# Optimization experiments

Measured on AMD Instinct MI355X. Metric: run time of the kernel, lower is better.

## Reference

```python
import jax, jax.numpy as jnp
import numpy as np

B, L, HID, NH = 4, 1024, 768, 12
D = HID // NH  # 64 per-head
SCALE = 1.0 / np.sqrt(D).astype(np.float32)
NEG = -1e15


def layer_norm(x, g, b, eps=1e-5):
    m = x.mean(-1, keepdims=True)
    v = ((x - m) ** 2).mean(-1, keepdims=True)
    return (x - m) / jnp.sqrt(v + eps) * g + b


def setup_inputs() -> dict:
    key = jax.random.key(0)
    ks = jax.random.split(key, 20)
    s = 0.02
    inp = jax.random.normal(ks[0], (B, L, HID), jnp.float32)
    seq_len = jax.random.randint(ks[1], (B,), 1, L + 1).astype(jnp.int32)
    rel_pos_embedding = jax.random.normal(ks[2], (B, NH, L, L), jnp.float32)
    def lin(k):
        k1, k2 = jax.random.split(k)
        W = jax.random.normal(k1, (HID, HID), jnp.float32) * s  # stored [in,out]
        b = jax.random.normal(k2, (HID,), jnp.float32) * s
        return W, b
    Wq, bq = lin(ks[3])
    Wk, bk = lin(ks[4])
    Wv, bv = lin(ks[5])
    Wo, bo = lin(ks[6])  # attn ff_final
    W0, b0 = lin(ks[7])  # FFN layer 0 (ff_size == hidden_size)
    W1, b1 = lin(ks[8])  # FFN layer 1
    ln_g = jnp.ones((HID,), jnp.float32)
    ln_b = jnp.zeros((HID,), jnp.float32)
    return {"inp": inp, "seq_len": seq_len, "lex_num": 0,
            "rel_pos_embedding": rel_pos_embedding,
            "Wq": Wq, "bq": bq, "Wk": Wk, "bk": bk, "Wv": Wv, "bv": bv,
            "Wo": Wo, "bo": bo, "W0": W0, "b0": b0, "W1": W1, "b1": b1,
            "ln_g": ln_g, "ln_b": ln_b}


def reference(inp, seq_len, lex_num, rel_pos_embedding,
              Wq, bq, Wk, bk, Wv, bv, Wo, bo, W0, b0, W1, b1, ln_g, ln_b):
    # layer_preprocess: '' -> identity
    x = inp
    # --- attention (q=k=v=x) ---
    q = (x @ Wq + bq).reshape(B, L, NH, D)
    k = (x @ Wk + bk).reshape(B, L, NH, D)
    v = (x @ Wv + bv).reshape(B, L, NH, D)
    scores = jnp.einsum('blhd,bmhd->bhlm', q, k) * SCALE + rel_pos_embedding
    valid = jnp.arange(L)[None, :] < (seq_len + lex_num)[:, None]  # [B,L]
    scores = jnp.where(valid[:, None, None, :], scores, NEG)
    attn = jax.nn.softmax(scores, axis=-1)  # attn dropout: eval mode -> identity
    ctx = jnp.einsum('bhlm,bmhd->blhd', attn, v).reshape(B, L, HID)
    y = ctx @ Wo + bo  # ff_final
    # layer_postprocess 'an': output = output + inp(of process); then LayerNorm
    y = layer_norm(y + y, ln_g, ln_b)
    # layer_preprocess '' -> identity, then FFN [hid, hid, hid]
    h = y @ W0 + b0
    h = jax.nn.relu(h)
    h = h @ W1 + b1
    out = layer_norm(h + h, ln_g, ln_b)
    return out
```

## Files before the change

kernel.cpp:

```cpp
#include <hip/hip_runtime.h>
#include <math.h>

#define B_   4
#define L_   1024
#define HID_ 768
#define NH_  12
#define D_   64
#define SCALE_ 0.125f
#define NEGV (-1e15f)

typedef __attribute__((ext_vector_type(4))) float  f32x4;
typedef __attribute__((ext_vector_type(8))) __bf16 bf16x8;
typedef __attribute__((ext_vector_type(8))) unsigned short ushort8v;
typedef __attribute__((ext_vector_type(4))) unsigned short ushort4v;

typedef const __attribute__((address_space(1))) unsigned int* gas1_t;
typedef __attribute__((address_space(3))) unsigned int*       las3_t;
#define GLDS16(g, l) __builtin_amdgcn_global_load_lds((gas1_t)(g), (las3_t)(l), 16, 0, 0)

static __device__ __forceinline__ unsigned short f2bf(float f) {
    unsigned int u = __builtin_bit_cast(unsigned int, f);
    u += 0x7fffu + ((u >> 16) & 1u);
    return (unsigned short)(u >> 16);
}

__global__ __launch_bounds__(256) void convert_x_kernel(
    const float* __restrict__ in, unsigned short* __restrict__ out, int n4)
{
    int i = blockIdx.x * 256 + threadIdx.x;
    if (i < n4) {
        float4 v = reinterpret_cast<const float4*>(in)[i];
        ushort4v o;
        o.x = f2bf(v.x); o.y = f2bf(v.y); o.z = f2bf(v.z); o.w = f2bf(v.w);
        reinterpret_cast<ushort4v*>(out)[i] = o;
    }
}

struct WArgs { const float* w[6]; unsigned short* wt[6]; };

__global__ __launch_bounds__(256) void transpose_w_kernel(WArgs a)
{
    const float* W = a.w[blockIdx.z];
    unsigned short* Wt = a.wt[blockIdx.z];
    __shared__ float t[64][65];
    const int tid = threadIdx.x;
    const int lr = tid >> 2, lc4 = (tid & 3) * 16;
    const int r0 = blockIdx.y * 64, c0 = blockIdx.x * 64;
#pragma unroll
    for (int j = 0; j < 4; ++j) {
        float4 v = *reinterpret_cast<const float4*>(&W[(size_t)(r0 + lr) * HID_ + c0 + lc4 + j * 4]);
        t[lr][lc4 + j * 4 + 0] = v.x;
        t[lr][lc4 + j * 4 + 1] = v.y;
        t[lr][lc4 + j * 4 + 2] = v.z;
        t[lr][lc4 + j * 4 + 3] = v.w;
    }
    __syncthreads();
    unsigned short tmp[16];
#pragma unroll
    for (int j = 0; j < 16; ++j) tmp[j] = f2bf(t[lc4 + j][lr]);
    unsigned short* dst = &Wt[(size_t)(c0 + lr) * HID_ + r0 + lc4];
    *reinterpret_cast<ushort8v*>(dst)     = *reinterpret_cast<ushort8v*>(&tmp[0]);
    *reinterpret_cast<ushort8v*>(dst + 8) = *reinterpret_cast<ushort8v*>(&tmp[8]);
}

struct GemmJob {
    const unsigned short* A;
    const unsigned short* Wt;
    const float* bias;
    void* C;
    int mode;
    int relu;
    float scale;
};
struct GemmArgs { GemmJob j[3]; };

__global__ __launch_bounds__(256, 4) void gemm_bf16_kernel(GemmArgs args)
{
    const GemmJob jb = args.j[blockIdx.z];
    __shared__ unsigned short As[64 * 64];
    __shared__ unsigned short Bs[128 * 64];

    const int tid = threadIdx.x;
    const int w = tid >> 6, lane = tid & 63, g = lane >> 4, lq = lane & 15;
    const int m0 = blockIdx.x * 64, n0 = blockIdx.y * 128;

    f32x4 acc[4][2];
#pragma unroll
    for (int i = 0; i < 4; ++i)
#pragma unroll
        for (int j = 0; j < 2; ++j) acc[i][j] = (f32x4){0.f, 0.f, 0.f, 0.f};

    const int sr = tid >> 3;
    const int kq = ((tid & 7) ^ (sr & 7)) * 8;
    const unsigned short* Ap0 = jb.A  + (size_t)(m0 + sr) * HID_ + kq;
    const unsigned short* Ap1 = jb.A  + (size_t)(m0 + 32 + sr) * HID_ + kq;
    const unsigned short* Bp0 = jb.Wt + (size_t)(n0 + sr) * HID_ + kq;
    const unsigned short* Bp1 = jb.Wt + (size_t)(n0 + 32 + sr) * HID_ + kq;
    const unsigned short* Bp2 = jb.Wt + (size_t)(n0 + 64 + sr) * HID_ + kq;
    const unsigned short* Bp3 = jb.Wt + (size_t)(n0 + 96 + sr) * HID_ + kq;
    char* AsB = (char*)As;
    char* BsB = (char*)Bs;
    const int wb = w * 1024;

    for (int k0 = 0; k0 < HID_; k0 += 64) {
        __syncthreads();
        GLDS16(Ap0 + k0, AsB + wb);
        GLDS16(Ap1 + k0, AsB + 4096 + wb);
        GLDS16(Bp0 + k0, BsB + wb);
        GLDS16(Bp1 + k0, BsB + 4096 + wb);
        GLDS16(Bp2 + k0, BsB + 8192 + wb);
        GLDS16(Bp3 + k0, BsB + 12288 + wb);
        __syncthreads();

#pragma unroll
        for (int ks = 0; ks < 2; ++ks) {
            bf16x8 af[4], bf[2];
#pragma unroll
            for (int mi = 0; mi < 4; ++mi) {
                int row = mi * 16 + lq;
                int c = (ks * 4 + g) ^ (row & 7);
                af[mi] = *reinterpret_cast<const bf16x8*>(&As[row * 64 + c * 8]);
            }
#pragma unroll
            for (int ni = 0; ni < 2; ++ni) {
                int row = w * 32 + ni * 16 + lq;
                int c = (ks * 4 + g) ^ (row & 7);
                bf[ni] = *reinterpret_cast<const bf16x8*>(&Bs[row * 64 + c * 8]);
            }
            __builtin_amdgcn_s_setprio(1);
#pragma unroll
            for (int mi = 0; mi < 4; ++mi)
#pragma unroll
                for (int ni = 0; ni < 2; ++ni)
                    acc[mi][ni] = __builtin_amdgcn_mfma_f32_16x16x32_bf16(
                        af[mi], bf[ni], acc[mi][ni], 0, 0, 0);
            __builtin_amdgcn_s_setprio(0);
        }
    }

    float bcol[2];
#pragma unroll
    for (int ni = 0; ni < 2; ++ni) bcol[ni] = jb.bias[n0 + w * 32 + ni * 16 + lq];

#pragma unroll
    for (int mi = 0; mi < 4; ++mi) {
#pragma unroll
        for (int ni = 0; ni < 2; ++ni) {
            const int n = n0 + w * 32 + ni * 16 + lq;
            float v[4];
#pragma unroll
            for (int r = 0; r < 4; ++r) {
                float x = (acc[mi][ni][r] + bcol[ni]) * jb.scale;
                if (jb.relu) x = fmaxf(x, 0.f);
                v[r] = x;
            }
            const int mbase = m0 + mi * 16 + 4 * g;
            if (jb.mode == 0) {
                float* C = (float*)jb.C;
#pragma unroll
                for (int r = 0; r < 4; ++r)
                    C[(size_t)(mbase + r) * HID_ + n] = v[r];
            } else if (jb.mode == 1) {
                unsigned short* C = (unsigned short*)jb.C;
#pragma unroll
                for (int r = 0; r < 4; ++r)
                    C[(size_t)(mbase + r) * HID_ + n] = f2bf(v[r]);
            } else {
                unsigned short* C = (unsigned short*)jb.C;
                const int bb = mbase >> 10, ltok = mbase & 1023;
                ushort4v o;
                o.x = f2bf(v[0]); o.y = f2bf(v[1]); o.z = f2bf(v[2]); o.w = f2bf(v[3]);
                *reinterpret_cast<ushort4v*>(&C[(size_t)(bb * HID_ + n) * L_ + ltok]) = o;
            }
        }
    }
}

__global__ __launch_bounds__(256, 3) void attn_mfma_kernel(
    const unsigned short* __restrict__ Qb, const unsigned short* __restrict__ Kb,
    const unsigned short* __restrict__ Vtb, const float* __restrict__ rel,
    const int* __restrict__ seq_len, const int* __restrict__ lex_num,
    unsigned short* __restrict__ ctx)
{
    const int qt = blockIdx.x, bh = blockIdx.y;
    const int b = bh / NH_, h = bh % NH_;
    const int q0 = qt * 64;
    const int sl = seq_len[b] + lex_num[0];
    const int nkt = (sl + 63) >> 6;

    __shared__ unsigned short Ks0[64 * 72], Ks1[64 * 72];
    __shared__ unsigned short Vs0[64 * 72], Vs1[64 * 72];
    __shared__ unsigned short Ps[64 * 72];

    const int tid = threadIdx.x;
    const int w = tid >> 6, lane = tid & 63, g = lane >> 4, lq = lane & 15;
    const int r0 = tid >> 3, cc0 = tid & 7;
    const int r1 = 32 + r0;

    const unsigned short* Kbase = Kb  + (size_t)(b * L_) * HID_ + h * D_;
    const unsigned short* Vbase = Vtb + (size_t)(b * HID_ + h * D_) * L_;
    const float* relbase = rel + (size_t)bh * (L_ * L_) + (size_t)(q0 + w * 16 + 4 * g) * L_ + lq;

    bf16x8 aq[2];
#pragma unroll
    for (int ks = 0; ks < 2; ++ks)
        aq[ks] = *reinterpret_cast<const bf16x8*>(
            &Qb[(size_t)(b * L_ + q0 + w * 16 + lq) * HID_ + h * D_ + ks * 32 + g * 8]);

    f32x4 acc[4];
    float m_r[4], l_r[4];
#pragma unroll
    for (int i = 0; i < 4; ++i) {
        acc[i] = (f32x4){0.f, 0.f, 0.f, 0.f};
        m_r[i] = -3e38f; l_r[i] = 0.f;
    }

    ushort8v kA0, kA1, vA0, vA1, kB0, kB1, vB0, vB1;
    float relA[16], relB[16];

    auto load_set = [&](int kt_, ushort8v& K0, ushort8v& K1, ushort8v& V0,
                        ushort8v& V1, float (&R)[16]) {
        const int k0 = kt_ * 64;
        K0 = *reinterpret_cast<const ushort8v*>(&Kbase[(size_t)(k0 + r0) * HID_ + cc0 * 8]);
        K1 = *reinterpret_cast<const ushort8v*>(&Kbase[(size_t)(k0 + r1) * HID_ + cc0 * 8]);
        V0 = *reinterpret_cast<const ushort8v*>(&Vbase[(size_t)r0 * L_ + k0 + cc0 * 8]);
        V1 = *reinterpret_cast<const ushort8v*>(&Vbase[(size_t)r1 * L_ + k0 + cc0 * 8]);
#pragma unroll
        for (int ni = 0; ni < 4; ++ni)
#pragma unroll
            for (int r = 0; r < 4; ++r)
                R[ni * 4 + r] = relbase[(size_t)r * L_ + k0 + ni * 16];
    };

    auto body = [&](int kt_, ushort8v& K0, ushort8v& K1, ushort8v& V0, ushort8v& V1,
                    float (&R)[16], unsigned short* KsC, unsigned short* VsC) {
        const int k0 = kt_ * 64;
        *reinterpret_cast<ushort8v*>(&KsC[r0 * 72 + cc0 * 8]) = K0;
        *reinterpret_cast<ushort8v*>(&KsC[r1 * 72 + cc0 * 8]) = K1;
        *reinterpret_cast<ushort8v*>(&VsC[r0 * 72 + cc0 * 8]) = V0;
        *reinterpret_cast<ushort8v*>(&VsC[r1 * 72 + cc0 * 8]) = V1;
        __syncthreads();

        {
            int tn = kt_ + 2; if (tn > nkt - 1) tn = nkt - 1;
            const int kn = tn * 64;
            K0 = *reinterpret_cast<const ushort8v*>(&Kbase[(size_t)(kn + r0) * HID_ + cc0 * 8]);
            K1 = *reinterpret_cast<const ushort8v*>(&Kbase[(size_t)(kn + r1) * HID_ + cc0 * 8]);
            V0 = *reinterpret_cast<const ushort8v*>(&Vbase[(size_t)r0 * L_ + kn + cc0 * 8]);
            V1 = *reinterpret_cast<const ushort8v*>(&Vbase[(size_t)r1 * L_ + kn + cc0 * 8]);
        }

        f32x4 s[4];
#pragma unroll
        for (int ni = 0; ni < 4; ++ni) s[ni] = (f32x4){0.f, 0.f, 0.f, 0.f};
        __builtin_amdgcn_s_setprio(1);
#pragma unroll
        for (int ks = 0; ks < 2; ++ks) {
#pragma unroll
            for (int ni = 0; ni < 4; ++ni) {
                bf16x8 bk = *reinterpret_cast<const bf16x8*>(
                    &KsC[(ni * 16 + lq) * 72 + ks * 32 + g * 8]);
                s[ni] = __builtin_amdgcn_mfma_f32_16x16x32_bf16(aq[ks], bk, s[ni], 0, 0, 0);
            }
        }
        __builtin_amdgcn_s_setprio(0);

        float sv[4][4];
#pragma unroll
        for (int ni = 0; ni < 4; ++ni) {
            const int col = k0 + ni * 16 + lq;
            const bool ok = col < sl;
#pragma unroll
            for (int r = 0; r < 4; ++r)
                sv[ni][r] = ok ? (s[ni][r] + R[ni * 4 + r]) : NEGV;
        }

        {
            int tn = kt_ + 2; if (tn > nkt - 1) tn = nkt - 1;
            const int kn = tn * 64;
#pragma unroll
            for (int ni = 0; ni < 4; ++ni)
#pragma unroll
                for (int r = 0; r < 4; ++r)
                    R[ni * 4 + r] = relbase[(size_t)r * L_ + kn + ni * 16];
        }

#pragma unroll
        for (int r = 0; r < 4; ++r) {
            float rm = fmaxf(fmaxf(sv[0][r], sv[1][r]), fmaxf(sv[2][r], sv[3][r]));
            rm = fmaxf(rm, __shfl_xor(rm, 1, 16));
            rm = fmaxf(rm, __shfl_xor(rm, 2, 16));
            rm = fmaxf(rm, __shfl_xor(rm, 4, 16));
            rm = fmaxf(rm, __shfl_xor(rm, 8, 16));
            float mn = fmaxf(m_r[r], rm);
            float sc = __expf(m_r[r] - mn);
            float p[4], rs = 0.f;
#pragma unroll
            for (int ni = 0; ni < 4; ++ni) {
                p[ni] = __expf(sv[ni][r] - mn);
                rs += p[ni];
            }
            rs += __shfl_xor(rs, 1, 16);
            rs += __shfl_xor(rs, 2, 16);
            rs += __shfl_xor(rs, 4, 16);
            rs += __shfl_xor(rs, 8, 16);
            l_r[r] = l_r[r] * sc + rs;
            m_r[r] = mn;
#pragma unroll
            for (int ni = 0; ni < 4; ++ni) {
                acc[ni][r] *= sc;
                Ps[(w * 16 + 4 * g + r) * 72 + ni * 16 + lq] = f2bf(p[ni]);
            }
        }

        __builtin_amdgcn_s_setprio(1);
#pragma unroll
        for (int ks = 0; ks < 2; ++ks) {
            bf16x8 ap = *reinterpret_cast<const bf16x8*>(
                &Ps[(w * 16 + lq) * 72 + ks * 32 + g * 8]);
#pragma unroll
            for (int ni = 0; ni < 4; ++ni) {
                bf16x8 bv = *reinterpret_cast<const bf16x8*>(
                    &VsC[(ni * 16 + lq) * 72 + ks * 32 + g * 8]);
                acc[ni] = __builtin_amdgcn_mfma_f32_16x16x32_bf16(ap, bv, acc[ni], 0, 0, 0);
            }
        }
        __builtin_amdgcn_s_setprio(0);
    };

    load_set(0, kA0, kA1, vA0, vA1, relA);
    load_set(nkt > 1 ? 1 : 0, kB0, kB1, vB0, vB1, relB);

    for (int kt = 0; kt < nkt; kt += 2) {
        body(kt, kA0, kA1, vA0, vA1, relA, Ks0, Vs0);
        if (kt + 1 < nkt)
            body(kt + 1, kB0, kB1, vB0, vB1, relB, Ks1, Vs1);
    }

    float inv[4];
#pragma unroll
    for (int r = 0; r < 4; ++r) inv[r] = 1.f / l_r[r];
#pragma unroll
    for (int ni = 0; ni < 4; ++ni)
#pragma unroll
        for (int r = 0; r < 4; ++r)
            ctx[(size_t)(b * L_ + q0 + w * 16 + 4 * g + r) * HID_ + h * D_ + ni * 16 + lq] =
                f2bf(acc[ni][r] * inv[r]);
}

__global__ __launch_bounds__(256) void ln2_kernel(
    const float* __restrict__ in, const float* __restrict__ g,
    const float* __restrict__ bta, void* __restrict__ out, int bf16out)
{
    const int row = blockIdx.x;
    const float* x = in + (size_t)row * HID_;
    const int tid = threadIdx.x;

    float vals[3];
    float s = 0.f, ss = 0.f;
#pragma unroll
    for (int j = 0; j < 3; ++j) {
        float t = 2.f * x[tid + j * 256];
        vals[j] = t;
        s += t;
        ss += t * t;
    }
#pragma unroll
    for (int m = 1; m < 64; m <<= 1) {
        s += __shfl_xor(s, m, 64);
        ss += __shfl_xor(ss, m, 64);
    }
    __shared__ float sb[4], ssb[4];
    if ((tid & 63) == 0) { sb[tid >> 6] = s; ssb[tid >> 6] = ss; }
    __syncthreads();
    s = sb[0] + sb[1] + sb[2] + sb[3];
    ss = ssb[0] + ssb[1] + ssb[2] + ssb[3];
    const float mean = s * (1.f / 768.f);
    float var = ss * (1.f / 768.f) - mean * mean;
    if (var < 0.f) var = 0.f;
    const float invs = rsqrtf(var + 1e-5f);
    if (bf16out) {
        unsigned short* o = (unsigned short*)out;
#pragma unroll
        for (int j = 0; j < 3; ++j) {
            int c = tid + j * 256;
            o[(size_t)row * HID_ + c] = f2bf((vals[j] - mean) * invs * g[c] + bta[c]);
        }
    } else {
        float* o = (float*)out;
#pragma unroll
        for (int j = 0; j < 3; ++j) {
            int c = tid + j * 256;
            o[(size_t)row * HID_ + c] = (vals[j] - mean) * invs * g[c] + bta[c];
        }
    }
}

extern "C" void kernel_launch(void* const* d_in, const int* in_sizes, int n_in,
                              void* d_out, int out_size, void* d_ws, size_t ws_size,
                              hipStream_t stream) {
    const float* inp     = (const float*)d_in[0];
    const int*   seq_len = (const int*)d_in[1];
    const int*   lex_num = (const int*)d_in[2];
    const float* rel     = (const float*)d_in[3];
    const float* Wq = (const float*)d_in[4];
    const float* bq = (const float*)d_in[5];
    const float* Wk = (const float*)d_in[6];
    const float* bk = (const float*)d_in[7];
    const float* Wv = (const float*)d_in[8];
    const float* bv = (const float*)d_in[9];
    const float* Wo = (const float*)d_in[10];
    const float* bo = (const float*)d_in[11];
    const float* W0 = (const float*)d_in[12];
    const float* b0 = (const float*)d_in[13];
    const float* W1 = (const float*)d_in[14];
    const float* b1 = (const float*)d_in[15];
    const float* ln_g = (const float*)d_in[16];
    const float* ln_b = (const float*)d_in[17];
    float* out = (float*)d_out;

    char* W = (char*)d_ws;
    const size_t WT_SZ = (size_t)HID_ * HID_ * 2;
    unsigned short* Wt[6];
    for (int i = 0; i < 6; ++i) Wt[i] = (unsigned short*)(W + i * WT_SZ);
    size_t off = 6 * WT_SZ;
    const size_t TOK_BF = (size_t)B_ * L_ * HID_ * 2;
    unsigned short* qb  = (unsigned short*)(W + off); off += TOK_BF;
    unsigned short* kb  = (unsigned short*)(W + off); off += TOK_BF;
    unsigned short* vtb = (unsigned short*)(W + off); off += TOK_BF;
    unsigned short* Eb  = (unsigned short*)(W + off); off += TOK_BF;
    float* Fbuf = (float*)(W + off);

    unsigned short* Xb   = Eb;
    unsigned short* ctxb = Eb;
    unsigned short* y2b  = vtb;
    unsigned short* hb   = qb;

    convert_x_kernel<<<dim3(3072), dim3(256), 0, stream>>>(inp, Xb, (B_ * L_ * HID_) / 4);

    {
        WArgs wa;
        const float* ws_[6] = {Wq, Wk, Wv, Wo, W0, W1};
        for (int i = 0; i < 6; ++i) { wa.w[i] = ws_[i]; wa.wt[i] = Wt[i]; }
        transpose_w_kernel<<<dim3(12, 12, 6), dim3(256), 0, stream>>>(wa);
    }

    {
        GemmArgs ga;
        ga.j[0] = {Xb, Wt[0], bq, (void*)qb,  1, 0, SCALE_};
        ga.j[1] = {Xb, Wt[1], bk, (void*)kb,  1, 0, 1.f};
        ga.j[2] = {Xb, Wt[2], bv, (void*)vtb, 2, 0, 1.f};
        gemm_bf16_kernel<<<dim3(64, 6, 3), dim3(256), 0, stream>>>(ga);
    }

    attn_mfma_kernel<<<dim3(16, 48), dim3(256), 0, stream>>>(
        qb, kb, vtb, rel, seq_len, lex_num, ctxb);

    {
        GemmArgs ga;
        ga.j[0] = {ctxb, Wt[3], bo, (void*)Fbuf, 0, 0, 1.f};
        gemm_bf16_kernel<<<dim3(64, 6, 1), dim3(256), 0, stream>>>(ga);
    }
    ln2_kernel<<<dim3(4096), dim3(256), 0, stream>>>(Fbuf, ln_g, ln_b, (void*)y2b, 1);
    {
        GemmArgs ga;
        ga.j[0] = {y2b, Wt[4], b0, (void*)hb, 1, 1, 1.f};
        gemm_bf16_kernel<<<dim3(64, 6, 1), dim3(256), 0, stream>>>(ga);
    }
    {
        GemmArgs ga;
        ga.j[0] = {hb, Wt[5], b1, (void*)Fbuf, 0, 0, 1.f};
        gemm_bf16_kernel<<<dim3(64, 6, 1), dim3(256), 0, stream>>>(ga);
    }
    ln2_kernel<<<dim3(4096), dim3(256), 0, stream>>>(Fbuf, ln_g, ln_b, (void*)out, 0);
}
```

Baseline: 132.8 us.

## Stage attention K/V tiles via direct global-to-LDS loads with XOR-swizzled layout

The attention kernel no longer loads K and V tiles into registers and then writes them to shared memory. It now uses global_load_lds to copy them straight into double-buffered, unpadded LDS tiles, and the MFMA operand reads use an XOR swizzle to avoid bank conflicts. The pipeline is rewritten with explicit s_barrier calls, a sched_barrier and a hand-set s_waitcnt vmcnt(36), so the next tile's K/V and rel-pos loads stay in flight while the current tile is computed. This cuts register pressure and VALU/LDS store work, but it depends on a hard-coded outstanding-load count that must match the exact number of issued loads.

```diff
diff --git a/kernel.cpp b/kernel.cpp
--- a/kernel.cpp
+++ b/kernel.cpp
@@ -187,18 +187,25 @@
     const int q0 = qt * 64;
     const int sl = seq_len[b] + lex_num[0];
     const int nkt = (sl + 63) >> 6;
-
-    __shared__ unsigned short Ks0[64 * 72], Ks1[64 * 72];
-    __shared__ unsigned short Vs0[64 * 72], Vs1[64 * 72];
+    const int ktmax = nkt - 1;
+
+    __shared__ unsigned short Ks[2][64 * 64];
+    __shared__ unsigned short Vs[2][64 * 64];
     __shared__ unsigned short Ps[64 * 72];
 
     const int tid = threadIdx.x;
     const int w = tid >> 6, lane = tid & 63, g = lane >> 4, lq = lane & 15;
-    const int r0 = tid >> 3, cc0 = tid & 7;
-    const int r1 = 32 + r0;
-
+    const int wb = w * 1024;
+
+    const int rS0 = tid >> 3,      sw0 = ((tid & 7) ^ (rS0 & 7)) * 8;
+    const int rS1 = 32 + (tid >> 3), sw1 = ((tid & 7) ^ (rS1 & 7)) * 8;
     const unsigned short* Kbase = Kb  + (size_t)(b * L_) * HID_ + h * D_;
     const unsigned short* Vbase = Vtb + (size_t)(b * HID_ + h * D_) * L_;
+    const unsigned short* Kc0 = Kbase + (size_t)rS0 * HID_ + sw0;
+    const unsigned short* Kc1 = Kbase + (size_t)rS1 * HID_ + sw1;
+    const unsigned short* Vc0 = Vbase + (size_t)rS0 * L_ + sw0;
+    const unsigned short* Vc1 = Vbase + (size_t)rS1 * L_ + sw1;
+
     const float* relbase = rel + (size_t)bh * (L_ * L_) + (size_t)(q0 + w * 16 + 4 * g) * L_ + lq;
 
     bf16x8 aq[2];
@@ -215,16 +222,19 @@
         m_r[i] = -3e38f; l_r[i] = 0.f;
     }
 
-    ushort8v kA0, kA1, vA0, vA1, kB0, kB1, vB0, vB1;
     float relA[16], relB[16];
 
-    auto load_set = [&](int kt_, ushort8v& K0, ushort8v& K1, ushort8v& V0,
-                        ushort8v& V1, float (&R)[16]) {
-        const int k0 = kt_ * 64;
-        K0 = *reinterpret_cast<const ushort8v*>(&Kbase[(size_t)(k0 + r0) * HID_ + cc0 * 8]);
-        K1 = *reinterpret_cast<const ushort8v*>(&Kbase[(size_t)(k0 + r1) * HID_ + cc0 * 8]);
-        V0 = *reinterpret_cast<const ushort8v*>(&Vbase[(size_t)r0 * L_ + k0 + cc0 * 8]);
-        V1 = *reinterpret_cast<const ushort8v*>(&Vbase[(size_t)r1 * L_ + k0 + cc0 * 8]);
+    auto stage = [&](int kt_, int p) {
+        const size_t k0 = (size_t)kt_ * 64;
+        char* KsB = (char*)Ks[p];
+        char* VsB = (char*)Vs[p];
+        GLDS16(Kc0 + k0 * HID_, KsB + wb);
+        GLDS16(Kc1 + k0 * HID_, KsB + 4096 + wb);
+        GLDS16(Vc0 + k0,        VsB + wb);
+        GLDS16(Vc1 + k0,        VsB + 4096 + wb);
+    };
+    auto loadrel = [&](int kt_, float (&R)[16]) {
+        const size_t k0 = (size_t)kt_ * 64;
 #pragma unroll
         for (int ni = 0; ni < 4; ++ni)
 #pragma unroll
@@ -232,23 +242,10 @@
                 R[ni * 4 + r] = relbase[(size_t)r * L_ + k0 + ni * 16];
     };
 
-    auto body = [&](int kt_, ushort8v& K0, ushort8v& K1, ushort8v& V0, ushort8v& V1,
-                    float (&R)[16], unsigned short* KsC, unsigned short* VsC) {
+    auto compute = [&](int kt_, int p, float (&R)[16]) {
         const int k0 = kt_ * 64;
-        *reinterpret_cast<ushort8v*>(&KsC[r0 * 72 + cc0 * 8]) = K0;
-        *reinterpret_cast<ushort8v*>(&KsC[r1 * 72 + cc0 * 8]) = K1;
-        *reinterpret_cast<ushort8v*>(&VsC[r0 * 72 + cc0 * 8]) = V0;
-        *reinterpret_cast<ushort8v*>(&VsC[r1 * 72 + cc0 * 8]) = V1;
-        __syncthreads();
-
-        {
-            int tn = kt_ + 2; if (tn > nkt - 1) tn = nkt - 1;
-            const int kn = tn * 64;
-            K0 = *reinterpret_cast<const ushort8v*>(&Kbase[(size_t)(kn + r0) * HID_ + cc0 * 8]);
-            K1 = *reinterpret_cast<const ushort8v*>(&Kbase[(size_t)(kn + r1) * HID_ + cc0 * 8]);
-            V0 = *reinterpret_cast<const ushort8v*>(&Vbase[(size_t)r0 * L_ + kn + cc0 * 8]);
-            V1 = *reinterpret_cast<const ushort8v*>(&Vbase[(size_t)r1 * L_ + kn + cc0 * 8]);
-        }
+        const char* KsB = (const char*)Ks[p];
+        const char* VsB = (const char*)Vs[p];
 
         f32x4 s[4];
 #pragma unroll
@@ -259,7 +256,7 @@
 #pragma unroll
             for (int ni = 0; ni < 4; ++ni) {
                 bf16x8 bk = *reinterpret_cast<const bf16x8*>(
-                    &KsC[(ni * 16 + lq) * 72 + ks * 32 + g * 8]);
+                    KsB + (ni * 16 + lq) * 128 + (((ks * 4 + g) ^ (lq & 7)) * 16));
                 s[ni] = __builtin_amdgcn_mfma_f32_16x16x32_bf16(aq[ks], bk, s[ni], 0, 0, 0);
             }
         }
@@ -273,16 +270,6 @@
 #pragma unroll
             for (int r = 0; r < 4; ++r)
                 sv[ni][r] = ok ? (s[ni][r] + R[ni * 4 + r]) : NEGV;
-        }
-
-        {
-            int tn = kt_ + 2; if (tn > nkt - 1) tn = nkt - 1;
-            const int kn = tn * 64;
-#pragma unroll
-            for (int ni = 0; ni < 4; ++ni)
-#pragma unroll
-                for (int r = 0; r < 4; ++r)
-                    R[ni * 4 + r] = relbase[(size_t)r * L_ + kn + ni * 16];
         }
 
 #pragma unroll
@@ -294,11 +281,11 @@
             rm = fmaxf(rm, __shfl_xor(rm, 8, 16));
             float mn = fmaxf(m_r[r], rm);
             float sc = __expf(m_r[r] - mn);
-            float p[4], rs = 0.f;
+            float p_[4], rs = 0.f;
 #pragma unroll
             for (int ni = 0; ni < 4; ++ni) {
-                p[ni] = __expf(sv[ni][r] - mn);
-                rs += p[ni];
+                p_[ni] = __expf(sv[ni][r] - mn);
+                rs += p_[ni];
             }
             rs += __shfl_xor(rs, 1, 16);
             rs += __shfl_xor(rs, 2, 16);
@@ -309,7 +296,7 @@
 #pragma unroll
             for (int ni = 0; ni < 4; ++ni) {
                 acc[ni][r] *= sc;
-                Ps[(w * 16 + 4 * g + r) * 72 + ni * 16 + lq] = f2bf(p[ni]);
+                Ps[(w * 16 + 4 * g + r) * 72 + ni * 16 + lq] = f2bf(p_[ni]);
             }
         }
 
@@ -321,20 +308,37 @@
 #pragma unroll
             for (int ni = 0; ni < 4; ++ni) {
                 bf16x8 bv = *reinterpret_cast<const bf16x8*>(
-                    &VsC[(ni * 16 + lq) * 72 + ks * 32 + g * 8]);
+                    VsB + (ni * 16 + lq) * 128 + (((ks * 4 + g) ^ (lq & 7)) * 16));
                 acc[ni] = __builtin_amdgcn_mfma_f32_16x16x32_bf16(ap, bv, acc[ni], 0, 0, 0);
             }
         }
         __builtin_amdgcn_s_setprio(0);
     };
 
-    load_set(0, kA0, kA1, vA0, vA1, relA);
-    load_set(nkt > 1 ? 1 : 0, kB0, kB1, vB0, vB1, relB);
+    stage(0, 0);
+    loadrel(0, relA);
 
     for (int kt = 0; kt < nkt; kt += 2) {
-        body(kt, kA0, kA1, vA0, vA1, relA, Ks0, Vs0);
-        if (kt + 1 < nkt)
-            body(kt + 1, kB0, kB1, vB0, vB1, relB, Ks1, Vs1);
+        {
+            int tn = kt + 1 > ktmax ? ktmax : kt + 1;
+            __builtin_amdgcn_s_barrier();
+            stage(tn, 1);
+            loadrel(tn, relB);
+            __builtin_amdgcn_sched_barrier(0);
+            asm volatile("s_waitcnt vmcnt(36)" ::: "memory");
+            __builtin_amdgcn_s_barrier();
+            compute(kt, 0, relA);
+        }
+        if (kt + 1 < nkt) {
+            int tn = kt + 2 > ktmax ? ktmax : kt + 2;
+            __builtin_amdgcn_s_barrier();
+            stage(tn, 0);
+            loadrel(tn, relA);
+            __builtin_amdgcn_sched_barrier(0);
+            asm volatile("s_waitcnt vmcnt(36)" ::: "memory");
+            __builtin_amdgcn_s_barrier();
+            compute(kt + 1, 1, relB);
+        }
     }
 
     float inv[4];
```

After: 137.7 us. +3.7%, slower.

## Use 128-key tiles with direct global-to-LDS loads in attention

Applied to the files above, without the earlier changes.

The attention kernel now processes 128 keys per iteration instead of 64. K and V tiles are loaded straight into shared memory with global_load_lds, replacing the register-staged, double-buffered prefetch of K, V and the relative-position bias. The aim is fewer loop iterations and barriers and less register pressure. In exchange, the prefetch overlap is gone, so load latency and rel-bias reads sit in each iteration's critical path. The new unpadded LDS layout may also cause bank conflicts on the K and V fragment reads.

```diff
diff --git a/kernel.cpp b/kernel.cpp
--- a/kernel.cpp
+++ b/kernel.cpp
@@ -186,19 +186,23 @@
     const int b = bh / NH_, h = bh % NH_;
     const int q0 = qt * 64;
     const int sl = seq_len[b] + lex_num[0];
-    const int nkt = (sl + 63) >> 6;
-
-    __shared__ unsigned short Ks0[64 * 72], Ks1[64 * 72];
-    __shared__ unsigned short Vs0[64 * 72], Vs1[64 * 72];
-    __shared__ unsigned short Ps[64 * 72];
+    const int nkt = (sl + 127) >> 7;
+
+    __shared__ unsigned short Ks[128 * 64];
+    __shared__ unsigned short Vs[64 * 128];
+    __shared__ unsigned short Ps[64 * 136];
 
     const int tid = threadIdx.x;
     const int w = tid >> 6, lane = tid & 63, g = lane >> 4, lq = lane & 15;
-    const int r0 = tid >> 3, cc0 = tid & 7;
-    const int r1 = 32 + r0;
-
+
+    const int rK = tid >> 3, cK = (tid & 7) * 8;
+    const int rV = tid >> 4, cV = (tid & 15) * 8;
     const unsigned short* Kbase = Kb  + (size_t)(b * L_) * HID_ + h * D_;
     const unsigned short* Vbase = Vtb + (size_t)(b * HID_ + h * D_) * L_;
+    char* KsB = (char*)Ks;
+    char* VsB = (char*)Vs;
+    const int wb = w * 1024;
+
     const float* relbase = rel + (size_t)bh * (L_ * L_) + (size_t)(q0 + w * 16 + 4 * g) * L_ + lq;
 
     bf16x8 aq[2];
@@ -215,88 +219,64 @@
         m_r[i] = -3e38f; l_r[i] = 0.f;
     }
 
-    ushort8v kA0, kA1, vA0, vA1, kB0, kB1, vB0, vB1;
-    float relA[16], relB[16];
-
-    auto load_set = [&](int kt_, ushort8v& K0, ushort8v& K1, ushort8v& V0,
-                        ushort8v& V1, float (&R)[16]) {
-        const int k0 = kt_ * 64;
-        K0 = *reinterpret_cast<const ushort8v*>(&Kbase[(size_t)(k0 + r0) * HID_ + cc0 * 8]);
-        K1 = *reinterpret_cast<const ushort8v*>(&Kbase[(size_t)(k0 + r1) * HID_ + cc0 * 8]);
-        V0 = *reinterpret_cast<const ushort8v*>(&Vbase[(size_t)r0 * L_ + k0 + cc0 * 8]);
-        V1 = *reinterpret_cast<const ushort8v*>(&Vbase[(size_t)r1 * L_ + k0 + cc0 * 8]);
-#pragma unroll
-        for (int ni = 0; ni < 4; ++ni)
+    for (int kt = 0; kt < nkt; ++kt) {
+        const int k0 = kt * 128;
+        __syncthreads();
+
+#pragma unroll
+        for (int j = 0; j < 4; ++j)
+            GLDS16(&Kbase[(size_t)(k0 + j * 32 + rK) * HID_ + cK], KsB + j * 4096 + wb);
+#pragma unroll
+        for (int j = 0; j < 4; ++j)
+            GLDS16(&Vbase[(size_t)(j * 16 + rV) * L_ + k0 + cV], VsB + j * 4096 + wb);
+
+        float rv[8][4];
+#pragma unroll
+        for (int ni = 0; ni < 8; ++ni)
 #pragma unroll
             for (int r = 0; r < 4; ++r)
-                R[ni * 4 + r] = relbase[(size_t)r * L_ + k0 + ni * 16];
-    };
-
-    auto body = [&](int kt_, ushort8v& K0, ushort8v& K1, ushort8v& V0, ushort8v& V1,
-                    float (&R)[16], unsigned short* KsC, unsigned short* VsC) {
-        const int k0 = kt_ * 64;
-        *reinterpret_cast<ushort8v*>(&KsC[r0 * 72 + cc0 * 8]) = K0;
-        *reinterpret_cast<ushort8v*>(&KsC[r1 * 72 + cc0 * 8]) = K1;
-        *reinterpret_cast<ushort8v*>(&VsC[r0 * 72 + cc0 * 8]) = V0;
-        *reinterpret_cast<ushort8v*>(&VsC[r1 * 72 + cc0 * 8]) = V1;
+                rv[ni][r] = relbase[(size_t)r * L_ + k0 + ni * 16];
+
         __syncthreads();
 
-        {
-            int tn = kt_ + 2; if (tn > nkt - 1) tn = nkt - 1;
-            const int kn = tn * 64;
-            K0 = *reinterpret_cast<const ushort8v*>(&Kbase[(size_t)(kn + r0) * HID_ + cc0 * 8]);
-            K1 = *reinterpret_cast<const ushort8v*>(&Kbase[(size_t)(kn + r1) * HID_ + cc0 * 8]);
-            V0 = *reinterpret_cast<const ushort8v*>(&Vbase[(size_t)r0 * L_ + kn + cc0 * 8]);
-            V1 = *reinterpret_cast<const ushort8v*>(&Vbase[(size_t)r1 * L_ + kn + cc0 * 8]);
-        }
-
-        f32x4 s[4];
-#pragma unroll
-        for (int ni = 0; ni < 4; ++ni) s[ni] = (f32x4){0.f, 0.f, 0.f, 0.f};
+        f32x4 s[8];
+#pragma unroll
+        for (int ni = 0; ni < 8; ++ni) s[ni] = (f32x4){0.f, 0.f, 0.f, 0.f};
         __builtin_amdgcn_s_setprio(1);
 #pragma unroll
-        for (int ks = 0; ks < 2; ++ks) {
-#pragma unroll
-            for (int ni = 0; ni < 4; ++ni) {
+        for (int ks = 0; ks < 2; ++ks)
+#pragma unroll
+            for (int ni = 0; ni < 8; ++ni) {
                 bf16x8 bk = *reinterpret_cast<const bf16x8*>(
-                    &KsC[(ni * 16 + lq) * 72 + ks * 32 + g * 8]);
+                    &Ks[(ni * 16 + lq) * 64 + ks * 32 + g * 8]);
                 s[ni] = __builtin_amdgcn_mfma_f32_16x16x32_bf16(aq[ks], bk, s[ni], 0, 0, 0);
             }
-        }
         __builtin_amdgcn_s_setprio(0);
 
-        float sv[4][4];
-#pragma unroll
-        for (int ni = 0; ni < 4; ++ni) {
+        float sv[8][4];
+#pragma unroll
+        for (int ni = 0; ni < 8; ++ni) {
             const int col = k0 + ni * 16 + lq;
             const bool ok = col < sl;
 #pragma unroll
             for (int r = 0; r < 4; ++r)
-                sv[ni][r] = ok ? (s[ni][r] + R[ni * 4 + r]) : NEGV;
-        }
-
-        {
-            int tn = kt_ + 2; if (tn > nkt - 1) tn = nkt - 1;
-            const int kn = tn * 64;
-#pragma unroll
-            for (int ni = 0; ni < 4; ++ni)
-#pragma unroll
-                for (int r = 0; r < 4; ++r)
-                    R[ni * 4 + r] = relbase[(size_t)r * L_ + kn + ni * 16];
+                sv[ni][r] = ok ? (s[ni][r] + rv[ni][r]) : NEGV;
         }
 
 #pragma unroll
         for (int r = 0; r < 4; ++r) {
-            float rm = fmaxf(fmaxf(sv[0][r], sv[1][r]), fmaxf(sv[2][r], sv[3][r]));
+            float rm = sv[0][r];
+#pragma unroll
+            for (int ni = 1; ni < 8; ++ni) rm = fmaxf(rm, sv[ni][r]);
             rm = fmaxf(rm, __shfl_xor(rm, 1, 16));
             rm = fmaxf(rm, __shfl_xor(rm, 2, 16));
             rm = fmaxf(rm, __shfl_xor(rm, 4, 16));
             rm = fmaxf(rm, __shfl_xor(rm, 8, 16));
             float mn = fmaxf(m_r[r], rm);
             float sc = __expf(m_r[r] - mn);
-            float p[4], rs = 0.f;
-#pragma unroll
-            for (int ni = 0; ni < 4; ++ni) {
+            float p[8], rs = 0.f;
+#pragma unroll
+            for (int ni = 0; ni < 8; ++ni) {
                 p[ni] = __expf(sv[ni][r] - mn);
                 rs += p[ni];
             }
@@ -307,34 +287,25 @@
             l_r[r] = l_r[r] * sc + rs;
             m_r[r] = mn;
 #pragma unroll
-            for (int ni = 0; ni < 4; ++ni) {
-                acc[ni][r] *= sc;
-                Ps[(w * 16 + 4 * g + r) * 72 + ni * 16 + lq] = f2bf(p[ni]);
-            }
+            for (int ni = 0; ni < 4; ++ni) acc[ni][r] *= sc;
+#pragma unroll
+            for (int ni = 0; ni < 8; ++ni)
+                Ps[(w * 16 + 4 * g + r) * 136 + ni * 16 + lq] = f2bf(p[ni]);
         }
 
         __builtin_amdgcn_s_setprio(1);
 #pragma unroll
-        for (int ks = 0; ks < 2; ++ks) {
+        for (int ks = 0; ks < 4; ++ks) {
             bf16x8 ap = *reinterpret_cast<const bf16x8*>(
-                &Ps[(w * 16 + lq) * 72 + ks * 32 + g * 8]);
+                &Ps[(w * 16 + lq) * 136 + ks * 32 + g * 8]);
 #pragma unroll
             for (int ni = 0; ni < 4; ++ni) {
                 bf16x8 bv = *reinterpret_cast<const bf16x8*>(
-                    &VsC[(ni * 16 + lq) * 72 + ks * 32 + g * 8]);
+                    &Vs[(ni * 16 + lq) * 128 + ks * 32 + g * 8]);
                 acc[ni] = __builtin_amdgcn_mfma_f32_16x16x32_bf16(ap, bv, acc[ni], 0, 0, 0);
             }
         }
         __builtin_amdgcn_s_setprio(0);
-    };
-
-    load_set(0, kA0, kA1, vA0, vA1, relA);
-    load_set(nkt > 1 ? 1 : 0, kB0, kB1, vB0, vB1, relB);
-
-    for (int kt = 0; kt < nkt; kt += 2) {
-        body(kt, kA0, kA1, vA0, vA1, relA, Ks0, Vs0);
-        if (kt + 1 < nkt)
-            body(kt + 1, kB0, kB1, vB0, vB1, relB, Ks1, Vs1);
     }
 
     float inv[4];
```

After: 142.3 us. +7.2%, slower.

## Transpose attention MFMA outputs so each lane owns one query row

Applied to the files above, without the earlier changes.

Swaps the MFMA A/B operands in both the QK^T and PV products so the accumulator is transposed: each lane now holds four consecutive key columns of a single query row. As a result the rel_pos bias loads become 16-byte vector loads instead of 16 strided scalar loads. The softmax row statistics reduce to one max/sum per lane with two cross-lane shuffles, and the P and ctx stores become 4-wide vector writes. It changes the fragment layout that the P tile and output stores depend on, so correctness relies on the transposed-accumulator indexing being consistent.

```diff
diff --git a/kernel.cpp b/kernel.cpp
--- a/kernel.cpp
+++ b/kernel.cpp
@@ -199,7 +199,7 @@
 
     const unsigned short* Kbase = Kb  + (size_t)(b * L_) * HID_ + h * D_;
     const unsigned short* Vbase = Vtb + (size_t)(b * HID_ + h * D_) * L_;
-    const float* relbase = rel + (size_t)bh * (L_ * L_) + (size_t)(q0 + w * 16 + 4 * g) * L_ + lq;
+    const float* relbase = rel + (size_t)bh * (L_ * L_) + (size_t)(q0 + w * 16 + lq) * L_ + 4 * g;
 
     bf16x8 aq[2];
 #pragma unroll
@@ -208,18 +208,15 @@
             &Qb[(size_t)(b * L_ + q0 + w * 16 + lq) * HID_ + h * D_ + ks * 32 + g * 8]);
 
     f32x4 acc[4];
-    float m_r[4], l_r[4];
-#pragma unroll
-    for (int i = 0; i < 4; ++i) {
-        acc[i] = (f32x4){0.f, 0.f, 0.f, 0.f};
-        m_r[i] = -3e38f; l_r[i] = 0.f;
-    }
+#pragma unroll
+    for (int i = 0; i < 4; ++i) acc[i] = (f32x4){0.f, 0.f, 0.f, 0.f};
+    float m_r = -3e38f, l_r = 0.f;
 
     ushort8v kA0, kA1, vA0, vA1, kB0, kB1, vB0, vB1;
-    float relA[16], relB[16];
+    f32x4 relA[4], relB[4];
 
     auto load_set = [&](int kt_, ushort8v& K0, ushort8v& K1, ushort8v& V0,
-                        ushort8v& V1, float (&R)[16]) {
+                        ushort8v& V1, f32x4 (&R)[4]) {
         const int k0 = kt_ * 64;
         K0 = *reinterpret_cast<const ushort8v*>(&Kbase[(size_t)(k0 + r0) * HID_ + cc0 * 8]);
         K1 = *reinterpret_cast<const ushort8v*>(&Kbase[(size_t)(k0 + r1) * HID_ + cc0 * 8]);
@@ -227,13 +224,11 @@
         V1 = *reinterpret_cast<const ushort8v*>(&Vbase[(size_t)r1 * L_ + k0 + cc0 * 8]);
 #pragma unroll
         for (int ni = 0; ni < 4; ++ni)
-#pragma unroll
-            for (int r = 0; r < 4; ++r)
-                R[ni * 4 + r] = relbase[(size_t)r * L_ + k0 + ni * 16];
+            R[ni] = *reinterpret_cast<const f32x4*>(&relbase[k0 + ni * 16]);
     };
 
     auto body = [&](int kt_, ushort8v& K0, ushort8v& K1, ushort8v& V0, ushort8v& V1,
-                    float (&R)[16], unsigned short* KsC, unsigned short* VsC) {
+                    f32x4 (&R)[4], unsigned short* KsC, unsigned short* VsC) {
         const int k0 = kt_ * 64;
         *reinterpret_cast<ushort8v*>(&KsC[r0 * 72 + cc0 * 8]) = K0;
         *reinterpret_cast<ushort8v*>(&KsC[r1 * 72 + cc0 * 8]) = K1;
@@ -260,7 +255,7 @@
             for (int ni = 0; ni < 4; ++ni) {
                 bf16x8 bk = *reinterpret_cast<const bf16x8*>(
                     &KsC[(ni * 16 + lq) * 72 + ks * 32 + g * 8]);
-                s[ni] = __builtin_amdgcn_mfma_f32_16x16x32_bf16(aq[ks], bk, s[ni], 0, 0, 0);
+                s[ni] = __builtin_amdgcn_mfma_f32_16x16x32_bf16(bk, aq[ks], s[ni], 0, 0, 0);
             }
         }
         __builtin_amdgcn_s_setprio(0);
@@ -268,11 +263,10 @@
         float sv[4][4];
 #pragma unroll
         for (int ni = 0; ni < 4; ++ni) {
-            const int col = k0 + ni * 16 + lq;
-            const bool ok = col < sl;
+            const int colb = k0 + ni * 16 + 4 * g;
 #pragma unroll
             for (int r = 0; r < 4; ++r)
-                sv[ni][r] = ok ? (s[ni][r] + R[ni * 4 + r]) : NEGV;
+                sv[ni][r] = (colb + r < sl) ? (s[ni][r] + R[ni][r]) : NEGV;
         }
 
         {
@@ -280,37 +274,40 @@
             const int kn = tn * 64;
 #pragma unroll
             for (int ni = 0; ni < 4; ++ni)
-#pragma unroll
-                for (int r = 0; r < 4; ++r)
-                    R[ni * 4 + r] = relbase[(size_t)r * L_ + kn + ni * 16];
-        }
-
-#pragma unroll
-        for (int r = 0; r < 4; ++r) {
-            float rm = fmaxf(fmaxf(sv[0][r], sv[1][r]), fmaxf(sv[2][r], sv[3][r]));
-            rm = fmaxf(rm, __shfl_xor(rm, 1, 16));
-            rm = fmaxf(rm, __shfl_xor(rm, 2, 16));
-            rm = fmaxf(rm, __shfl_xor(rm, 4, 16));
-            rm = fmaxf(rm, __shfl_xor(rm, 8, 16));
-            float mn = fmaxf(m_r[r], rm);
-            float sc = __expf(m_r[r] - mn);
-            float p[4], rs = 0.f;
-#pragma unroll
-            for (int ni = 0; ni < 4; ++ni) {
-                p[ni] = __expf(sv[ni][r] - mn);
-                rs += p[ni];
-            }
-            rs += __shfl_xor(rs, 1, 16);
-            rs += __shfl_xor(rs, 2, 16);
-            rs += __shfl_xor(rs, 4, 16);
-            rs += __shfl_xor(rs, 8, 16);
-            l_r[r] = l_r[r] * sc + rs;
-            m_r[r] = mn;
-#pragma unroll
-            for (int ni = 0; ni < 4; ++ni) {
-                acc[ni][r] *= sc;
-                Ps[(w * 16 + 4 * g + r) * 72 + ni * 16 + lq] = f2bf(p[ni]);
-            }
+                R[ni] = *reinterpret_cast<const f32x4*>(&relbase[kn + ni * 16]);
+        }
+
+        float rm = sv[0][0];
+#pragma unroll
+        for (int ni = 0; ni < 4; ++ni)
+#pragma unroll
+            for (int r = 0; r < 4; ++r) rm = fmaxf(rm, sv[ni][r]);
+        rm = fmaxf(rm, __shfl_xor(rm, 16));
+        rm = fmaxf(rm, __shfl_xor(rm, 32));
+        const float mn = fmaxf(m_r, rm);
+        const float sc = __expf(m_r - mn);
+        float p[4][4];
+        float rs = 0.f;
+#pragma unroll
+        for (int ni = 0; ni < 4; ++ni)
+#pragma unroll
+            for (int r = 0; r < 4; ++r) {
+                p[ni][r] = __expf(sv[ni][r] - mn);
+                rs += p[ni][r];
+            }
+        rs += __shfl_xor(rs, 16);
+        rs += __shfl_xor(rs, 32);
+        l_r = l_r * sc + rs;
+        m_r = mn;
+#pragma unroll
+        for (int ni = 0; ni < 4; ++ni) acc[ni] *= sc;
+
+#pragma unroll
+        for (int ni = 0; ni < 4; ++ni) {
+            ushort4v o;
+            o.x = f2bf(p[ni][0]); o.y = f2bf(p[ni][1]);
+            o.z = f2bf(p[ni][2]); o.w = f2bf(p[ni][3]);
+            *reinterpret_cast<ushort4v*>(&Ps[(w * 16 + lq) * 72 + ni * 16 + 4 * g]) = o;
         }
 
         __builtin_amdgcn_s_setprio(1);
@@ -322,7 +319,7 @@
             for (int ni = 0; ni < 4; ++ni) {
                 bf16x8 bv = *reinterpret_cast<const bf16x8*>(
                     &VsC[(ni * 16 + lq) * 72 + ks * 32 + g * 8]);
-                acc[ni] = __builtin_amdgcn_mfma_f32_16x16x32_bf16(ap, bv, acc[ni], 0, 0, 0);
+                acc[ni] = __builtin_amdgcn_mfma_f32_16x16x32_bf16(bv, ap, acc[ni], 0, 0, 0);
             }
         }
         __builtin_amdgcn_s_setprio(0);
@@ -337,15 +334,17 @@
             body(kt + 1, kB0, kB1, vB0, vB1, relB, Ks1, Vs1);
     }
 
-    float inv[4];
-#pragma unroll
-    for (int r = 0; r < 4; ++r) inv[r] = 1.f / l_r[r];
-#pragma unroll
-    for (int ni = 0; ni < 4; ++ni)
-#pragma unroll
-        for (int r = 0; r < 4; ++r)
-            ctx[(size_t)(b * L_ + q0 + w * 16 + 4 * g + r) * HID_ + h * D_ + ni * 16 + lq] =
-                f2bf(acc[ni][r] * inv[r]);
+    const float inv = 1.f / l_r;
+    unsigned short* cbase = ctx + (size_t)(b * L_ + q0 + w * 16 + lq) * HID_ + h * D_;
+#pragma unroll
+    for (int ni = 0; ni < 4; ++ni) {
+        ushort4v o;
+        o.x = f2bf(acc[ni][0] * inv);
+        o.y = f2bf(acc[ni][1] * inv);
+        o.z = f2bf(acc[ni][2] * inv);
+        o.w = f2bf(acc[ni][3] * inv);
+        *reinterpret_cast<ushort4v*>(&cbase[ni * 16 + 4 * g]) = o;
+    }
 }
 
 __global__ __launch_bounds__(256) void ln2_kernel(
```

New measurement: 129.2 us. 2.7% less time.
